# Kernel tuning notes

Measured on AMD Instinct MI355X. Metric: run time of the kernel, lower is better.

The kernel has to match this reference:

```python
import jax, jax.numpy as jnp
import numpy as np

N = 16384   # points (batch=1, divisible by patch_size so padding is identity)
C = 512     # channels
H = 8       # num_heads
K = 1024    # patch_size
G = 48      # voxel grid extent
EPS = 1e-5
SCALE = (C // H) ** -0.5


def setup_inputs() -> dict:
    rng = np.random.default_rng(0)
    # unique occupied voxels
    flat = rng.choice(G ** 3, size=N, replace=False)
    gx = flat // (G * G); gy = (flat // G) % G; gz = flat % G
    coords = np.stack([gx, gy, gz], 1).astype(np.int64)
    # occupancy LUT on padded grid -> neighbor index per 3x3x3 kernel offset (-1 = empty)
    lut = -np.ones(((G + 2) ** 3,), np.int64)
    def flt(c):
        return ((c[:, 0] + 1) * (G + 2) + (c[:, 1] + 1)) * (G + 2) + (c[:, 2] + 1)
    lut[flt(coords)] = np.arange(N)
    offs = np.array([[dx, dy, dz] for dx in (-1, 0, 1) for dy in (-1, 0, 1) for dz in (-1, 0, 1)], np.int64)
    nbr = np.stack([lut[flt(coords + o)] for o in offs], 1)  # [N,27]
    # Morton (z-order) serialization order
    def spread(v):
        v = v.astype(np.int64); r = np.zeros_like(v)
        for b in range(6):
            r |= ((v >> b) & 1) << (3 * b)
        return r
    code = (spread(gx) << 2) | (spread(gy) << 1) | spread(gz)
    order = np.argsort(code, kind='stable').astype(np.int32)

    key = jax.random.key(0)
    ks = jax.random.split(key, 8)
    s = 0.02
    p = lambda k, shape: jax.random.normal(k, shape, jnp.float32) * s
    return dict(
        feat=jax.random.normal(ks[0], (N, C), jnp.float32),
        neighbor_idx=jnp.asarray(nbr, jnp.int32),
        order=jnp.asarray(order, jnp.int32),
        cpe_w=p(ks[1], (27, C, C)), cpe_b=jnp.zeros((C,), jnp.float32),
        cpe_lin_w=p(ks[2], (C, C)), cpe_lin_b=jnp.zeros((C,), jnp.float32),
        cpe_ln_g=jnp.ones((C,), jnp.float32), cpe_ln_b=jnp.zeros((C,), jnp.float32),
        ln1_g=jnp.ones((C,), jnp.float32), ln1_b=jnp.zeros((C,), jnp.float32),
        qkv_w=p(ks[3], (3 * C, C)), qkv_b=jnp.zeros((3 * C,), jnp.float32),
        proj_w=p(ks[4], (C, C)), proj_b=jnp.zeros((C,), jnp.float32),
        ln2_g=jnp.ones((C,), jnp.float32), ln2_b=jnp.zeros((C,), jnp.float32),
        fc1_w=p(ks[5], (4 * C, C)), fc1_b=jnp.zeros((4 * C,), jnp.float32),
        fc2_w=p(ks[6], (C, 4 * C)), fc2_b=jnp.zeros((C,), jnp.float32),
    )


def _ln(x, g, b):
    m = x.mean(-1, keepdims=True)
    v = ((x - m) ** 2).mean(-1, keepdims=True)
    return (x - m) * jax.lax.rsqrt(v + EPS) * g + b


def _block(feat, neighbor_idx, order, cpe_w, cpe_b, cpe_lin_w, cpe_lin_b,
           cpe_ln_g, cpe_ln_b, ln1_g, ln1_b, qkv_w, qkv_b, proj_w, proj_b,
           ln2_g, ln2_b, fc1_w, fc1_b, fc2_w, fc2_b):
    # ---- CPE: SubMConv3d(3x3x3) -> Linear -> LayerNorm, residual ----
    valid = neighbor_idx >= 0
    idx = jnp.maximum(neighbor_idx, 0)
    h = jnp.zeros_like(feat)
    for kk in range(27):  # fixed kernel volume
        g = jnp.where(valid[:, kk:kk + 1], feat[idx[:, kk]], 0.0)
        h = h + g @ cpe_w[kk].T
    h = h + cpe_b
    h = h @ cpe_lin_w.T + cpe_lin_b
    h = _ln(h, cpe_ln_g, cpe_ln_b)
    feat = feat + h
    # ---- Serialized windowed attention (pre-norm, residual) ----
    x = _ln(feat, ln1_g, ln1_b)
    qkv = (x @ qkv_w.T + qkv_b)[order]                 # gather by serialized order
    qkv = qkv.reshape(N // K, K, 3, H, C // H)         # [P,K,3,H,hd]
    q = qkv[:, :, 0].transpose(0, 2, 1, 3)             # [P,H,K,hd]
    k = qkv[:, :, 1].transpose(0, 2, 1, 3)
    v = qkv[:, :, 2].transpose(0, 2, 1, 3)
    attn = jax.nn.softmax(jnp.einsum('phkd,phjd->phkj', q * SCALE, k), axis=-1)
    o = jnp.einsum('phkj,phjd->phkd', attn, v).transpose(0, 2, 1, 3).reshape(N, C)
    inverse = jnp.argsort(order)                       # scatter back
    o = o[inverse] @ proj_w.T + proj_b
    feat = feat + o
    # ---- MLP (pre-norm, residual) ----
    x = _ln(feat, ln2_g, ln2_b)
    x = jax.nn.gelu(x @ fc1_w.T + fc1_b, approximate=False)
    x = x @ fc2_w.T + fc2_b
    return feat + x


def reference(feat, neighbor_idx, order, cpe_w, cpe_b, cpe_lin_w, cpe_lin_b,
              cpe_ln_g, cpe_ln_b, ln1_g, ln1_b, qkv_w, qkv_b, proj_w, proj_b,
              ln2_g, ln2_b, fc1_w, fc1_b, fc2_w, fc2_b):
    return _block(feat, neighbor_idx, order, cpe_w, cpe_b, cpe_lin_w, cpe_lin_b,
                  cpe_ln_g, cpe_ln_b, ln1_g, ln1_b, qkv_w, qkv_b, proj_w, proj_b,
                  ln2_g, ln2_b, fc1_w, fc1_b, fc2_w, fc2_b)
```

## Files before the change

kernel.cpp:

```cpp
#include <hip/hip_runtime.h>
#include <math.h>

typedef unsigned short u16;
typedef unsigned int u32;
typedef unsigned long long u64;
typedef __attribute__((ext_vector_type(8))) short short8;
typedef __attribute__((ext_vector_type(4))) float f32x4;

#define NPTS 16384
#define MAXP 98304
#define MAXTILE 768

__device__ __forceinline__ u16 f2bf(float f) {
  u32 u = __float_as_uint(f);
  u = (u + 0x7fffu + ((u >> 16) & 1u)) >> 16;
  return (u16)u;
}
__device__ __forceinline__ float bf2f(u16 u) {
  return __uint_as_float((u32)u << 16);
}

__device__ __forceinline__ void gl2lds16(const u16* g, u16* l) {
  __builtin_amdgcn_global_load_lds(
      (const __attribute__((address_space(1))) u32*)g,
      (__attribute__((address_space(3))) u32*)l, 16, 0, 0);
}

__device__ __forceinline__ float wredsum(float v) {
#pragma unroll
  for (int m = 1; m < 64; m <<= 1) v += __shfl_xor(v, m, 64);
  return v;
}

__global__ void cvt_comb(const float* __restrict__ feat,
                         const float* __restrict__ w0, const float* __restrict__ w1,
                         const float* __restrict__ w2, const float* __restrict__ w3,
                         const float* __restrict__ w4, const float* __restrict__ w5,
                         u16* __restrict__ dst) {
  const int i = blockIdx.x * 256 + threadIdx.x;
  if (i >= 4718720) return;
  ushort4 o;
  if (i < 2097280) {
    if (i < 2097152) {
      float4 v = ((const float4*)feat)[i];
      o.x = f2bf(v.x); o.y = f2bf(v.y); o.z = f2bf(v.z); o.w = f2bf(v.w);
    } else {
      o.x = 0; o.y = 0; o.z = 0; o.w = 0;
    }
  } else {
    const int j = i - 2097280;
    const float* s;
    int li;
    if (j < 1769472) { s = w0; li = j; }
    else if (j < 1835008) { s = w1; li = j - 1769472; }
    else if (j < 2031616) { s = w2; li = j - 1835008; }
    else if (j < 2097152) { s = w3; li = j - 2031616; }
    else if (j < 2359296) { s = w4; li = j - 2097152; }
    else { s = w5; li = j - 2359296; }
    float4 v = ((const float4*)s)[li];
    o.x = f2bf(v.x); o.y = f2bf(v.y); o.z = f2bf(v.z); o.w = f2bf(v.w);
  }
  ((ushort4*)dst)[i] = o;
}

__global__ void mkinv(const int* __restrict__ order, int* __restrict__ inv) {
  int i = blockIdx.x * 256 + threadIdx.x;
  if (i < NPTS) inv[order[i]] = i;
}

__global__ __launch_bounds__(256) void cpe_cnt(const int* __restrict__ nbr,
                                               int* __restrict__ wcnt) {
  const int wglob = blockIdx.x * 4 + (threadIdx.x >> 6);
  const int lane = threadIdx.x & 63;
  const int i = wglob * 64 + lane;
  const int* row = nbr + i * 27;
#pragma unroll 1
  for (int kk = 0; kk < 27; kk++) {
    const u64 m = __ballot(row[kk] >= 0);
    if (lane == 0) wcnt[wglob * 27 + kk] = (int)__popcll(m);
  }
}

__global__ __launch_bounds__(256) void cpe_plan(
    const int* __restrict__ wcnt, int* __restrict__ chunkoff,
    int* __restrict__ off, int* __restrict__ tkk, int* __restrict__ meta,
    int* __restrict__ pairj) {
  __shared__ int s_cnt[27], s_off[27], s_ts[27], s_tk[27];
  const int tid = threadIdx.x;
  if (tid < 27) {
    int run = 0;
#pragma unroll 1
    for (int c = 0; c < 256; c++) {
      chunkoff[c * 27 + tid] = run;
      run += wcnt[c * 27 + tid];
    }
    s_cnt[tid] = run;
  }
  __syncthreads();
  if (tid == 0) {
    int pos = 0, t = 0;
#pragma unroll 1
    for (int kk = 0; kk < 27; kk++) {
      s_off[kk] = pos;
      off[kk] = pos;
      int tk = (s_cnt[kk] + 127) >> 7;
      if (pos + tk * 128 > MAXP) tk = (MAXP - pos) >> 7;
      s_ts[kk] = t;
      s_tk[kk] = tk;
      t += tk;
      pos += tk * 128;
    }
    meta[0] = t;
  }
  __syncthreads();
#pragma unroll 1
  for (int kk = 0; kk < 27; kk++) {
    const int ts = s_ts[kk], tk = s_tk[kk];
    for (int u = tid; u < tk; u += 256) tkk[ts + u] = kk;
    const int base = s_off[kk], total = s_cnt[kk], padded = tk * 128;
    for (int p2 = total + tid; p2 < padded; p2 += 256) pairj[base + p2] = NPTS;
  }
}

__global__ __launch_bounds__(256) void cpe_scat(
    const int* __restrict__ nbr, const int* __restrict__ chunkoff,
    const int* __restrict__ off, int* __restrict__ pairj,
    int* __restrict__ pairpos) {
  const int wglob = blockIdx.x * 4 + (threadIdx.x >> 6);
  const int lane = threadIdx.x & 63;
  const int i = wglob * 64 + lane;
  const int* row = nbr + i * 27;
  const u64 below = (1ull << lane) - 1ull;
#pragma unroll 1
  for (int kk = 0; kk < 27; kk++) {
    const int v = row[kk];
    const bool valid = v >= 0;
    const u64 m = __ballot(valid);
    int pp = -1;
    if (valid) {
      const int t = off[kk] + chunkoff[wglob * 27 + kk] + (int)__popcll(m & below);
      if (t < MAXP) { pairj[t] = v; pp = t; }
    }
    pairpos[i * 27 + kk] = pp;
  }
}

__global__ __launch_bounds__(256, 2) void gemm_pair(
    const u16* __restrict__ Abase, const u16* __restrict__ Bw,
    const int* __restrict__ meta, const int* __restrict__ tkk,
    const int* __restrict__ pairj, u16* __restrict__ outp) {
  const int L = blockIdx.x;
  const int tile = (L >> 5) * 8 + (L & 7);
  const int n0b = (L >> 3) & 3;
  if (tile >= meta[0]) return;
  __shared__ __align__(16) u16 sA[128 * 32];
  __shared__ __align__(16) u16 sB[128 * 32];
  const int tid = threadIdx.x;
  const int wave = tid >> 6, lane = tid & 63;
  const int quad = lane >> 4, tl = lane & 15;
  const int wr = wave >> 1, wc = wave & 1;
  const int p0 = tile * 128, n0 = n0b * 128;
  const int kk = tkk[tile];
  const int srow = lane >> 2, scol = lane & 3;

  int r[2]; int ca[2];
#pragma unroll
  for (int o = 0; o < 2; o++) {
    r[o] = wave * 32 + o * 16 + srow;
    const int sw = (r[o] + (r[o] >> 2)) & 3;
    ca[o] = (scol ^ sw) * 8;
  }
  const int j0 = pairj[p0 + r[0]];
  const int j1 = pairj[p0 + r[1]];
  const u16* a0 = Abase + (size_t)j0 * 512 + ca[0];
  const u16* a1 = Abase + (size_t)j1 * 512 + ca[1];
  const u16* b0 = Bw + (size_t)kk * 262144 + (size_t)(n0 + r[0]) * 512 + ca[0];
  const u16* b1 = Bw + (size_t)kk * 262144 + (size_t)(n0 + r[1]) * 512 + ca[1];
  u16* ldsA0 = &sA[(wave * 32) * 32];
  u16* ldsA1 = &sA[(wave * 32 + 16) * 32];
  u16* ldsB0 = &sB[(wave * 32) * 32];
  u16* ldsB1 = &sB[(wave * 32 + 16) * 32];

  f32x4 acc[4][4] = {};
#pragma unroll 1
  for (int kc = 0; kc < 512; kc += 32) {
    __syncthreads();
    gl2lds16(a0 + kc, ldsA0);
    gl2lds16(b0 + kc, ldsB0);
    gl2lds16(a1 + kc, ldsA1);
    gl2lds16(b1 + kc, ldsB1);
    __syncthreads();
    short8 fa[4], fb[4];
#pragma unroll
    for (int i = 0; i < 4; i++) {
      const int ra = wr * 64 + i * 16 + tl;
      fa[i] = *(const short8*)&sA[ra * 32 + ((quad ^ ((ra + (ra >> 2)) & 3)) * 8)];
      const int rb = wc * 64 + i * 16 + tl;
      fb[i] = *(const short8*)&sB[rb * 32 + ((quad ^ ((rb + (rb >> 2)) & 3)) * 8)];
    }
#pragma unroll
    for (int i = 0; i < 4; i++)
#pragma unroll
      for (int j = 0; j < 4; j++)
        acc[i][j] = __builtin_amdgcn_mfma_f32_16x16x32_bf16(fa[i], fb[j], acc[i][j], 0, 0, 0);
  }

#pragma unroll
  for (int i = 0; i < 4; i++) {
    const int pB = p0 + wr * 64 + i * 16 + quad * 4;
#pragma unroll
    for (int j = 0; j < 4; j++) {
      const int n = n0 + wc * 64 + j * 16 + tl;
      f32x4 c = acc[i][j];
#pragma unroll
      for (int rr = 0; rr < 4; rr++)
        outp[(size_t)(pB + rr) * 512 + n] = f2bf(c[rr]);
    }
  }
}

__global__ __launch_bounds__(256, 4) void cpe_reduce(
    const u16* __restrict__ outp, const int* __restrict__ pairpos,
    const float* __restrict__ bias, u16* __restrict__ h) {
  const int wave = threadIdx.x >> 6, lane = threadIdx.x & 63;
  const int i = blockIdx.x * 4 + wave;
  const int c = lane * 8;
  float acc[8];
  const float4 b0 = *(const float4*)(bias + c);
  const float4 b1 = *(const float4*)(bias + c + 4);
  acc[0] = b0.x; acc[1] = b0.y; acc[2] = b0.z; acc[3] = b0.w;
  acc[4] = b1.x; acc[5] = b1.y; acc[6] = b1.z; acc[7] = b1.w;
  const int* pp = pairpos + i * 27;
#pragma unroll 1
  for (int kk = 0; kk < 27; kk++) {
    const int pos = pp[kk];
    if (pos >= 0) {
      const u16* row = outp + (size_t)pos * 512 + c;
      ushort4 u0 = *(const ushort4*)row;
      ushort4 u1 = *(const ushort4*)(row + 4);
      acc[0] += bf2f(u0.x); acc[1] += bf2f(u0.y);
      acc[2] += bf2f(u0.z); acc[3] += bf2f(u0.w);
      acc[4] += bf2f(u1.x); acc[5] += bf2f(u1.y);
      acc[6] += bf2f(u1.z); acc[7] += bf2f(u1.w);
    }
  }
  ushort4 o0, o1;
  o0.x = f2bf(acc[0]); o0.y = f2bf(acc[1]); o0.z = f2bf(acc[2]); o0.w = f2bf(acc[3]);
  o1.x = f2bf(acc[4]); o1.y = f2bf(acc[5]); o1.z = f2bf(acc[6]); o1.w = f2bf(acc[7]);
  *(ushort4*)(h + (size_t)i * 512 + c) = o0;
  *(ushort4*)(h + (size_t)i * 512 + c + 4) = o1;
}

__global__ __launch_bounds__(256) void vtrans(const u16* __restrict__ vr,
                                              u16* __restrict__ vt) {
  __shared__ u16 t[64 * 72];
  const int bid = blockIdx.x;
  const int ph = bid >> 4, jt = bid & 15;
  const u16* src = vr + (size_t)ph * 65536 + jt * 64 * 64;
  u16* dst = vt + (size_t)ph * 65536 + jt * 64;
  const int tid = threadIdx.x;
  {
    const int j = tid >> 2, d0 = (tid & 3) * 16;
    uint4 w0 = *(const uint4*)(src + j * 64 + d0);
    uint4 w1 = *(const uint4*)(src + j * 64 + d0 + 8);
    *(uint4*)&t[j * 72 + d0] = w0;
    *(uint4*)&t[j * 72 + d0 + 8] = w1;
  }
  __syncthreads();
  {
    const int dr = tid >> 2, j0 = (tid & 3) * 16;
    u16 tmp[16];
#pragma unroll
    for (int e = 0; e < 16; e++) tmp[e] = t[(j0 + e) * 72 + dr];
    *(uint4*)(dst + (size_t)dr * 1024 + j0) = *(uint4*)&tmp[0];
    *(uint4*)(dst + (size_t)dr * 1024 + j0 + 8) = *(uint4*)&tmp[8];
  }
}

enum { EP_BF16 = 0, EP_QKV = 2, EP_RES = 3, EP_GELU = 4 };

template <int EP>
__global__ __launch_bounds__(256, 2) void gemm_nt(
    const u16* __restrict__ A, const u16* __restrict__ B, int M, int N, int K,
    const float* __restrict__ bias, float* __restrict__ outf,
    u16* __restrict__ outb, const float* __restrict__ res,
    const int* __restrict__ inv, u16* __restrict__ oq, u16* __restrict__ okk,
    u16* __restrict__ ov) {
  __shared__ __align__(16) u16 sA[128 * 32];
  __shared__ __align__(16) u16 sB[128 * 32];
  const int tid = threadIdx.x;
  const int wave = tid >> 6, lane = tid & 63;
  const int quad = lane >> 4, tl = lane & 15;
  const int wr = wave >> 1, wc = wave & 1;
  const int m0 = blockIdx.x * 128, n0 = blockIdx.y * 128;
  const int srow = lane >> 2, scol = lane & 3;

  f32x4 acc[4][4] = {};

  for (int kt = 0; kt < K; kt += 32) {
    __syncthreads();
#pragma unroll
    for (int o = 0; o < 2; o++) {
      const int r = wave * 32 + o * 16 + srow;
      const int sw = (r + (r >> 2)) & 3;
      const int ca = (scol ^ sw) * 8;
      gl2lds16(A + (size_t)(m0 + r) * K + kt + ca, &sA[(wave * 32 + o * 16) * 32]);
      gl2lds16(B + (size_t)(n0 + r) * K + kt + ca, &sB[(wave * 32 + o * 16) * 32]);
    }
    __syncthreads();
    short8 fa[4], fb[4];
#pragma unroll
    for (int i = 0; i < 4; i++) {
      const int ra = wr * 64 + i * 16 + tl;
      fa[i] = *(const short8*)&sA[ra * 32 + ((quad ^ ((ra + (ra >> 2)) & 3)) * 8)];
      const int rb = wc * 64 + i * 16 + tl;
      fb[i] = *(const short8*)&sB[rb * 32 + ((quad ^ ((rb + (rb >> 2)) & 3)) * 8)];
    }
#pragma unroll
    for (int i = 0; i < 4; i++)
#pragma unroll
      for (int j = 0; j < 4; j++)
        acc[i][j] = __builtin_amdgcn_mfma_f32_16x16x32_bf16(fa[i], fb[j], acc[i][j], 0, 0, 0);
  }

#pragma unroll
  for (int i = 0; i < 4; i++) {
    const int mB = m0 + wr * 64 + i * 16 + quad * 4;
#pragma unroll
    for (int j = 0; j < 4; j++) {
      const int n = n0 + wc * 64 + j * 16 + tl;
      const float bv = bias[n];
      f32x4 c = acc[i][j];
#pragma unroll
      for (int r = 0; r < 4; r++) {
        const int m = mB + r;
        float v = c[r] + bv;
        if (EP == EP_BF16) {
          outb[(size_t)m * N + n] = f2bf(v);
        } else if (EP == EP_RES) {
          outf[(size_t)m * N + n] = v + res[(size_t)m * N + n];
        } else if (EP == EP_GELU) {
          float g = 0.5f * v * (1.0f + erff(v * 0.70710678118654752f));
          outb[(size_t)m * N + n] = f2bf(g);
        } else if (EP == EP_QKV) {
          const int s = n >> 9, hh = (n >> 6) & 7, d = n & 63;
          const int pos = inv[m];
          const size_t base = (size_t)((pos >> 10) * 8 + hh) * 65536;
          const int jj = pos & 1023;
          if (s == 0) oq[base + (size_t)jj * 64 + d] = f2bf(v * 0.125f);
          else if (s == 1) okk[base + (size_t)jj * 64 + d] = f2bf(v);
          else ov[base + (size_t)jj * 64 + d] = f2bf(v);
        }
      }
    }
  }
}

__global__ __launch_bounds__(256, 2) void attn(
    const u16* __restrict__ qs, const u16* __restrict__ kk_s,
    const u16* __restrict__ vts, const int* __restrict__ order,
    u16* __restrict__ obf) {
  __shared__ __align__(16) u16 Qt[128 * 64];
  __shared__ __align__(16) u16 Kt[64 * 64];
  __shared__ __align__(16) u16 Vt[64 * 64];
  __shared__ __align__(16) u16 Pl[4][32 * 72];
  const int tid = threadIdx.x;
  const int wave = tid >> 6, lane = tid & 63;
  const int quad = lane >> 4, tl = lane & 15;
  const int bid = blockIdx.x;
  const int qt = bid >> 7, ph = bid & 127;
  const int p = ph >> 3, h = ph & 7;
  const size_t base = (size_t)ph * 65536;

  {
    const u16* Qg = qs + base + qt * 8192;
#pragma unroll
    for (int i = 0; i < 4; i++) {
      const int op = wave * 4 + i;
      const int r = op * 8 + (lane >> 3);
      const int c8 = ((lane & 7) ^ (r & 7)) * 8;
      gl2lds16(Qg + r * 64 + c8, &Qt[op * 512]);
    }
  }

  float ls[2][4] = {};
  f32x4 acco[2][4] = {};

  for (int kt = 0; kt < 16; kt++) {
    __syncthreads();
    const u16* Kg = kk_s + base + kt * 4096;
    const u16* Vg = vts + base + kt * 64;
#pragma unroll
    for (int i = 0; i < 2; i++) {
      const int op = wave * 2 + i;
      const int r = op * 8 + (lane >> 3);
      const int c8 = ((lane & 7) ^ (r & 7)) * 8;
      gl2lds16(Kg + r * 64 + c8, &Kt[op * 512]);
      gl2lds16(Vg + r * 1024 + c8, &Vt[op * 512]);
    }
    __syncthreads();

    f32x4 accs[2][4] = {};
#pragma unroll
    for (int kd = 0; kd < 2; kd++) {
      short8 qa[2], kb[4];
#pragma unroll
      for (int a = 0; a < 2; a++) {
        const int r = wave * 32 + a * 16 + tl;
        const int oct = (kd * 4 + quad) ^ (r & 7);
        qa[a] = *(const short8*)&Qt[r * 64 + oct * 8];
      }
#pragma unroll
      for (int b = 0; b < 4; b++) {
        const int r = b * 16 + tl;
        const int oct = (kd * 4 + quad) ^ (r & 7);
        kb[b] = *(const short8*)&Kt[r * 64 + oct * 8];
      }
#pragma unroll
      for (int a = 0; a < 2; a++)
#pragma unroll
        for (int b = 0; b < 4; b++)
          accs[a][b] = __builtin_amdgcn_mfma_f32_16x16x32_bf16(qa[a], kb[b], accs[a][b], 0, 0, 0);
    }

    u16* plw = &Pl[wave][0];
#pragma unroll
    for (int a = 0; a < 2; a++)
#pragma unroll
      for (int c = 0; c < 4; c++) {
#pragma unroll
        for (int r = 0; r < 4; r++) {
          const float pe = __expf(accs[a][c][r]);
          accs[a][c][r] = pe;
          ls[a][r] += pe;
          plw[(a * 16 + quad * 4 + r) * 72 + c * 16 + tl] = f2bf(pe);
        }
      }

#pragma unroll
    for (int k2 = 0; k2 < 2; k2++) {
      short8 pa[2], vb[4];
#pragma unroll
      for (int a = 0; a < 2; a++)
        pa[a] = *(const short8*)&plw[(a * 16 + tl) * 72 + k2 * 32 + quad * 8];
#pragma unroll
      for (int b = 0; b < 4; b++) {
        const int rb = b * 16 + tl;
        vb[b] = *(const short8*)&Vt[rb * 64 + (((k2 * 4 + quad) ^ (rb & 7)) * 8)];
      }
#pragma unroll
      for (int a = 0; a < 2; a++)
#pragma unroll
        for (int b = 0; b < 4; b++)
          acco[a][b] = __builtin_amdgcn_mfma_f32_16x16x32_bf16(pa[a], vb[b], acco[a][b], 0, 0, 0);
    }
  }

#pragma unroll
  for (int a = 0; a < 2; a++)
#pragma unroll
    for (int r = 0; r < 4; r++) {
#pragma unroll
      for (int mk = 1; mk < 16; mk <<= 1) ls[a][r] += __shfl_xor(ls[a][r], mk, 64);
    }

  const int q0 = p * 1024 + qt * 128 + wave * 32;
#pragma unroll
  for (int a = 0; a < 2; a++)
#pragma unroll
    for (int r = 0; r < 4; r++) {
      const int orig = order[q0 + a * 16 + quad * 4 + r];
      const float il = 1.0f / ls[a][r];
#pragma unroll
      for (int b = 0; b < 4; b++)
        obf[(size_t)orig * 512 + h * 64 + b * 16 + tl] = f2bf(acco[a][b][r] * il);
    }
}

__global__ __launch_bounds__(256, 4) void ln_fuse1(
    const u16* __restrict__ h2, const float* __restrict__ feat,
    const float* __restrict__ cg, const float* __restrict__ cb,
    const float* __restrict__ g1, const float* __restrict__ b1,
    float* __restrict__ feat1, u16* __restrict__ xbf) {
  const int wave = threadIdx.x >> 6, lane = threadIdx.x & 63;
  const size_t row = (size_t)blockIdx.x * 4 + wave;
  const int c0 = lane * 4, c1 = 256 + lane * 4;
  const u16* hr = h2 + row * 512;
  ushort4 ha = *(const ushort4*)(hr + c0);
  ushort4 hb = *(const ushort4*)(hr + c1);
  float h[8];
  h[0] = bf2f(ha.x); h[1] = bf2f(ha.y); h[2] = bf2f(ha.z); h[3] = bf2f(ha.w);
  h[4] = bf2f(hb.x); h[5] = bf2f(hb.y); h[6] = bf2f(hb.z); h[7] = bf2f(hb.w);
  float s = 0.0f, q = 0.0f;
#pragma unroll
  for (int i = 0; i < 8; i++) { s += h[i]; q += h[i] * h[i]; }
  s = wredsum(s); q = wredsum(q);
  const float mean = s * (1.0f / 512.0f);
  const float var = q * (1.0f / 512.0f) - mean * mean;
  const float rs = rsqrtf(var + 1e-5f);
  float4 ga = *(const float4*)(cg + c0), gb = *(const float4*)(cg + c1);
  float4 ba = *(const float4*)(cb + c0), bb = *(const float4*)(cb + c1);
  const float* fr = feat + row * 512;
  float4 fa = *(const float4*)(fr + c0), fb = *(const float4*)(fr + c1);
  float f[8];
  f[0] = fa.x + (h[0] - mean) * rs * ga.x + ba.x;
  f[1] = fa.y + (h[1] - mean) * rs * ga.y + ba.y;
  f[2] = fa.z + (h[2] - mean) * rs * ga.z + ba.z;
  f[3] = fa.w + (h[3] - mean) * rs * ga.w + ba.w;
  f[4] = fb.x + (h[4] - mean) * rs * gb.x + bb.x;
  f[5] = fb.y + (h[5] - mean) * rs * gb.y + bb.y;
  f[6] = fb.z + (h[6] - mean) * rs * gb.z + bb.z;
  f[7] = fb.w + (h[7] - mean) * rs * gb.w + bb.w;
  float* f1r = feat1 + row * 512;
  *(float4*)(f1r + c0) = make_float4(f[0], f[1], f[2], f[3]);
  *(float4*)(f1r + c1) = make_float4(f[4], f[5], f[6], f[7]);
  float s2 = 0.0f, q2 = 0.0f;
#pragma unroll
  for (int i = 0; i < 8; i++) { s2 += f[i]; q2 += f[i] * f[i]; }
  s2 = wredsum(s2); q2 = wredsum(q2);
  const float mean2 = s2 * (1.0f / 512.0f);
  const float var2 = q2 * (1.0f / 512.0f) - mean2 * mean2;
  const float rs2 = rsqrtf(var2 + 1e-5f);
  float4 g1a = *(const float4*)(g1 + c0), g1b = *(const float4*)(g1 + c1);
  float4 b1a = *(const float4*)(b1 + c0), b1b = *(const float4*)(b1 + c1);
  ushort4 o0, o1;
  o0.x = f2bf((f[0] - mean2) * rs2 * g1a.x + b1a.x);
  o0.y = f2bf((f[1] - mean2) * rs2 * g1a.y + b1a.y);
  o0.z = f2bf((f[2] - mean2) * rs2 * g1a.z + b1a.z);
  o0.w = f2bf((f[3] - mean2) * rs2 * g1a.w + b1a.w);
  o1.x = f2bf((f[4] - mean2) * rs2 * g1b.x + b1b.x);
  o1.y = f2bf((f[5] - mean2) * rs2 * g1b.y + b1b.y);
  o1.z = f2bf((f[6] - mean2) * rs2 * g1b.z + b1b.z);
  o1.w = f2bf((f[7] - mean2) * rs2 * g1b.w + b1b.w);
  *(ushort4*)(xbf + row * 512 + c0) = o0;
  *(ushort4*)(xbf + row * 512 + c1) = o1;
}

__global__ __launch_bounds__(256, 4) void ln_only(
    const float* __restrict__ x, const float* __restrict__ g,
    const float* __restrict__ b_, u16* __restrict__ o) {
  const int wave = threadIdx.x >> 6, lane = threadIdx.x & 63;
  const size_t row = (size_t)blockIdx.x * 4 + wave;
  const int c0 = lane * 4, c1 = 256 + lane * 4;
  const float* xr = x + row * 512;
  float4 a = *(const float4*)(xr + c0);
  float4 b = *(const float4*)(xr + c1);
  float s = a.x + a.y + a.z + a.w + b.x + b.y + b.z + b.w;
  float q = a.x * a.x + a.y * a.y + a.z * a.z + a.w * a.w +
            b.x * b.x + b.y * b.y + b.z * b.z + b.w * b.w;
  s = wredsum(s); q = wredsum(q);
  const float mean = s * (1.0f / 512.0f);
  const float var = q * (1.0f / 512.0f) - mean * mean;
  const float rs = rsqrtf(var + 1e-5f);
  float4 ga = *(const float4*)(g + c0), gb = *(const float4*)(g + c1);
  float4 ba = *(const float4*)(b_ + c0), bb = *(const float4*)(b_ + c1);
  ushort4 o0, o1;
  o0.x = f2bf((a.x - mean) * rs * ga.x + ba.x);
  o0.y = f2bf((a.y - mean) * rs * ga.y + ba.y);
  o0.z = f2bf((a.z - mean) * rs * ga.z + ba.z);
  o0.w = f2bf((a.w - mean) * rs * ga.w + ba.w);
  o1.x = f2bf((b.x - mean) * rs * gb.x + bb.x);
  o1.y = f2bf((b.y - mean) * rs * gb.y + bb.y);
  o1.z = f2bf((b.z - mean) * rs * gb.z + bb.z);
  o1.w = f2bf((b.w - mean) * rs * gb.w + bb.w);
  *(ushort4*)(o + row * 512 + c0) = o0;
  *(ushort4*)(o + row * 512 + c1) = o1;
}

extern "C" void kernel_launch(void* const* d_in, const int* in_sizes, int n_in,
                              void* d_out, int out_size, void* d_ws, size_t ws_size,
                              hipStream_t stream) {
  (void)in_sizes; (void)n_in; (void)out_size; (void)ws_size;
  const float* feat = (const float*)d_in[0];
  const int* nbr = (const int*)d_in[1];
  const int* order = (const int*)d_in[2];
  const float* cpe_w = (const float*)d_in[3];
  const float* cpe_b = (const float*)d_in[4];
  const float* cpe_lin_w = (const float*)d_in[5];
  const float* cpe_lin_b = (const float*)d_in[6];
  const float* cpe_ln_g = (const float*)d_in[7];
  const float* cpe_ln_b = (const float*)d_in[8];
  const float* ln1_g = (const float*)d_in[9];
  const float* ln1_b = (const float*)d_in[10];
  const float* qkv_w = (const float*)d_in[11];
  const float* qkv_b = (const float*)d_in[12];
  const float* proj_w = (const float*)d_in[13];
  const float* proj_b = (const float*)d_in[14];
  const float* ln2_g = (const float*)d_in[15];
  const float* ln2_b = (const float*)d_in[16];
  const float* fc1_w = (const float*)d_in[17];
  const float* fc1_b = (const float*)d_in[18];
  const float* fc2_w = (const float*)d_in[19];
  const float* fc2_b = (const float*)d_in[20];
  float* out = (float*)d_out;

  char* ws = (char*)d_ws;
  size_t off = 0;
  auto alloc = [&](size_t bytes) {
    char* p = ws + off;
    off += (bytes + 255) & ~(size_t)255;
    return p;
  };
  u16* featbf = (u16*)alloc((size_t)(NPTS + 1) * 512 * 2);
  u16* w_cpe = (u16*)alloc((size_t)27 * 512 * 512 * 2);
  u16* w_cl = (u16*)alloc((size_t)512 * 512 * 2);
  u16* w_qkv = (u16*)alloc((size_t)1536 * 512 * 2);
  u16* w_proj = (u16*)alloc((size_t)512 * 512 * 2);
  u16* w_fc1 = (u16*)alloc((size_t)2048 * 512 * 2);
  u16* w_fc2 = (u16*)alloc((size_t)512 * 2048 * 2);
  u16* hbf = (u16*)alloc((size_t)NPTS * 512 * 2);
  char* big = alloc((size_t)NPTS * 2048 * 2);
  float* feat1 = (float*)alloc((size_t)NPTS * 512 * 4);
  int* inv = (int*)alloc((size_t)NPTS * 4);
  int* offs = (int*)alloc(27 * 4);
  int* meta = (int*)alloc(256);
  int* tkk = (int*)alloc((size_t)(MAXTILE + 1) * 4);
  int* pairj = (int*)alloc((size_t)MAXP * 4);
  int* pairpos = (int*)alloc((size_t)NPTS * 27 * 4);
  int* wcnt = (int*)alloc((size_t)256 * 27 * 4);
  int* chunkoff = (int*)alloc((size_t)256 * 27 * 4);

  u16* out_pair = (u16*)big;
  u16* h2 = (u16*)big;
  u16* qsb = (u16*)big;
  u16* ksb = qsb + (size_t)NPTS * 512;
  u16* vrow = ksb + (size_t)NPTS * 512;
  u16* vtb = vrow + (size_t)NPTS * 512;
  u16* tbf = (u16*)big;
  u16* xbf = hbf;
  u16* obf = hbf;
  u16* x2bf = featbf;

  cvt_comb<<<dim3(18433), dim3(256), 0, stream>>>(feat, cpe_w, cpe_lin_w, qkv_w,
                                                  proj_w, fc1_w, fc2_w, featbf);
  mkinv<<<dim3(NPTS / 256), dim3(256), 0, stream>>>(order, inv);

  cpe_cnt<<<dim3(64), dim3(256), 0, stream>>>(nbr, wcnt);
  cpe_plan<<<dim3(1), dim3(256), 0, stream>>>(wcnt, chunkoff, offs, tkk, meta, pairj);
  cpe_scat<<<dim3(64), dim3(256), 0, stream>>>(nbr, chunkoff, offs, pairj, pairpos);
  gemm_pair<<<dim3(MAXTILE * 4), dim3(256), 0, stream>>>(featbf, w_cpe, meta, tkk,
                                                         pairj, out_pair);
  cpe_reduce<<<dim3(NPTS / 4), dim3(256), 0, stream>>>(out_pair, pairpos, cpe_b, hbf);

  gemm_nt<EP_BF16><<<dim3(128, 4), dim3(256), 0, stream>>>(
      hbf, w_cl, NPTS, 512, 512, cpe_lin_b, nullptr, h2, nullptr, nullptr,
      nullptr, nullptr, nullptr);
  ln_fuse1<<<dim3(NPTS / 4), dim3(256), 0, stream>>>(
      h2, feat, cpe_ln_g, cpe_ln_b, ln1_g, ln1_b, feat1, xbf);
  gemm_nt<EP_QKV><<<dim3(128, 12), dim3(256), 0, stream>>>(
      xbf, w_qkv, NPTS, 1536, 512, qkv_b, nullptr, nullptr, nullptr, inv,
      qsb, ksb, vrow);
  vtrans<<<dim3(2048), dim3(256), 0, stream>>>(vrow, vtb);
  attn<<<dim3(1024), dim3(256), 0, stream>>>(qsb, ksb, vtb, order, obf);
  gemm_nt<EP_RES><<<dim3(128, 4), dim3(256), 0, stream>>>(
      obf, w_proj, NPTS, 512, 512, proj_b, out, nullptr, feat1, nullptr,
      nullptr, nullptr, nullptr);
  ln_only<<<dim3(NPTS / 4), dim3(256), 0, stream>>>(out, ln2_g, ln2_b, x2bf);
  gemm_nt<EP_GELU><<<dim3(128, 16), dim3(256), 0, stream>>>(
      x2bf, w_fc1, NPTS, 2048, 512, fc1_b, nullptr, tbf, nullptr, nullptr,
      nullptr, nullptr, nullptr);
  gemm_nt<EP_RES><<<dim3(128, 4), dim3(256), 0, stream>>>(
      tbf, w_fc2, NPTS, 512, 2048, fc2_b, out, nullptr, out, nullptr,
      nullptr, nullptr, nullptr);
}
```

Measured before the change: 596.2 us.

## Halve tile sizes for attention and N=512 GEMMs to raise block count

Adds a 64x128-tile GEMM variant used for the cpe_lin, proj and fc2 GEMMs, doubling their grid to 1024 blocks. The attention kernel now handles 64 queries per block instead of 128, doubling blocks to 2048, with lower LDS and register use and a higher occupancy bound. The aim is to fill the GPU's many CUs better, since 512 blocks underfill the machine. The cost is reloading K/V tiles twice as often, lower arithmetic intensity per block, and a single-buffered k-loop with small 32-wide steps in the new GEMM.

```diff
diff --git a/kernel.cpp b/kernel.cpp
--- a/kernel.cpp
+++ b/kernel.cpp
@@ -356,14 +356,86 @@
   }
 }
 
-__global__ __launch_bounds__(256, 2) void attn(
+template <int EP>
+__global__ __launch_bounds__(256) void gemm_nt64(
+    const u16* __restrict__ A, const u16* __restrict__ B, int M, int N, int K,
+    const float* __restrict__ bias, float* __restrict__ outf,
+    u16* __restrict__ outb, const float* __restrict__ res) {
+  __shared__ __align__(16) u16 sA[64 * 32];
+  __shared__ __align__(16) u16 sB[128 * 32];
+  const int tid = threadIdx.x;
+  const int wave = tid >> 6, lane = tid & 63;
+  const int quad = lane >> 4, tl = lane & 15;
+  const int wr = wave >> 1, wc = wave & 1;
+  const int m0 = blockIdx.x * 64, n0 = blockIdx.y * 128;
+  const int srow = lane >> 2, scol = lane & 3;
+
+  f32x4 acc[2][4] = {};
+
+  for (int kt = 0; kt < K; kt += 32) {
+    __syncthreads();
+    {
+      const int r = wave * 16 + srow;
+      const int sw = (r + (r >> 2)) & 3;
+      const int ca = (scol ^ sw) * 8;
+      gl2lds16(A + (size_t)(m0 + r) * K + kt + ca, &sA[(wave * 16) * 32]);
+    }
+#pragma unroll
+    for (int o = 0; o < 2; o++) {
+      const int r = wave * 32 + o * 16 + srow;
+      const int sw = (r + (r >> 2)) & 3;
+      const int ca = (scol ^ sw) * 8;
+      gl2lds16(B + (size_t)(n0 + r) * K + kt + ca, &sB[(wave * 32 + o * 16) * 32]);
+    }
+    __syncthreads();
+    short8 fa[2], fb[4];
+#pragma unroll
+    for (int i = 0; i < 2; i++) {
+      const int ra = wr * 32 + i * 16 + tl;
+      fa[i] = *(const short8*)&sA[ra * 32 + ((quad ^ ((ra + (ra >> 2)) & 3)) * 8)];
+    }
+#pragma unroll
+    for (int j = 0; j < 4; j++) {
+      const int rb = wc * 64 + j * 16 + tl;
+      fb[j] = *(const short8*)&sB[rb * 32 + ((quad ^ ((rb + (rb >> 2)) & 3)) * 8)];
+    }
+#pragma unroll
+    for (int i = 0; i < 2; i++)
+#pragma unroll
+      for (int j = 0; j < 4; j++)
+        acc[i][j] = __builtin_amdgcn_mfma_f32_16x16x32_bf16(fa[i], fb[j], acc[i][j], 0, 0, 0);
+  }
+
+#pragma unroll
+  for (int i = 0; i < 2; i++) {
+    const int mB = m0 + wr * 32 + i * 16 + quad * 4;
+#pragma unroll
+    for (int j = 0; j < 4; j++) {
+      const int n = n0 + wc * 64 + j * 16 + tl;
+      const float bv = bias[n];
+      f32x4 c = acc[i][j];
+#pragma unroll
+      for (int r = 0; r < 4; r++) {
+        const int m = mB + r;
+        float v = c[r] + bv;
+        if (EP == EP_BF16) {
+          outb[(size_t)m * N + n] = f2bf(v);
+        } else if (EP == EP_RES) {
+          outf[(size_t)m * N + n] = v + res[(size_t)m * N + n];
+        }
+      }
+    }
+  }
+}
+
+__global__ __launch_bounds__(256, 4) void attn(
     const u16* __restrict__ qs, const u16* __restrict__ kk_s,
     const u16* __restrict__ vts, const int* __restrict__ order,
     u16* __restrict__ obf) {
-  __shared__ __align__(16) u16 Qt[128 * 64];
+  __shared__ __align__(16) u16 Qt[64 * 64];
   __shared__ __align__(16) u16 Kt[64 * 64];
   __shared__ __align__(16) u16 Vt[64 * 64];
-  __shared__ __align__(16) u16 Pl[4][32 * 72];
+  __shared__ __align__(16) u16 Pl[4][16 * 72];
   const int tid = threadIdx.x;
   const int wave = tid >> 6, lane = tid & 63;
   const int quad = lane >> 4, tl = lane & 15;
@@ -373,18 +445,18 @@
   const size_t base = (size_t)ph * 65536;
 
   {
-    const u16* Qg = qs + base + qt * 8192;
-#pragma unroll
-    for (int i = 0; i < 4; i++) {
-      const int op = wave * 4 + i;
+    const u16* Qg = qs + base + qt * 4096;
+#pragma unroll
+    for (int i = 0; i < 2; i++) {
+      const int op = wave * 2 + i;
       const int r = op * 8 + (lane >> 3);
       const int c8 = ((lane & 7) ^ (r & 7)) * 8;
       gl2lds16(Qg + r * 64 + c8, &Qt[op * 512]);
     }
   }
 
-  float ls[2][4] = {};
-  f32x4 acco[2][4] = {};
+  float ls[4] = {};
+  f32x4 acco[4] = {};
 
   for (int kt = 0; kt < 16; kt++) {
     __syncthreads();
@@ -400,15 +472,14 @@
     }
     __syncthreads();
 
-    f32x4 accs[2][4] = {};
+    f32x4 accs[4] = {};
 #pragma unroll
     for (int kd = 0; kd < 2; kd++) {
-      short8 qa[2], kb[4];
-#pragma unroll
-      for (int a = 0; a < 2; a++) {
-        const int r = wave * 32 + a * 16 + tl;
+      short8 qa, kb[4];
+      {
+        const int r = wave * 16 + tl;
         const int oct = (kd * 4 + quad) ^ (r & 7);
-        qa[a] = *(const short8*)&Qt[r * 64 + oct * 8];
+        qa = *(const short8*)&Qt[r * 64 + oct * 8];
       }
 #pragma unroll
       for (int b = 0; b < 4; b++) {
@@ -417,64 +488,52 @@
         kb[b] = *(const short8*)&Kt[r * 64 + oct * 8];
       }
 #pragma unroll
-      for (int a = 0; a < 2; a++)
-#pragma unroll
-        for (int b = 0; b < 4; b++)
-          accs[a][b] = __builtin_amdgcn_mfma_f32_16x16x32_bf16(qa[a], kb[b], accs[a][b], 0, 0, 0);
+      for (int b = 0; b < 4; b++)
+        accs[b] = __builtin_amdgcn_mfma_f32_16x16x32_bf16(qa, kb[b], accs[b], 0, 0, 0);
     }
 
     u16* plw = &Pl[wave][0];
 #pragma unroll
-    for (int a = 0; a < 2; a++)
-#pragma unroll
-      for (int c = 0; c < 4; c++) {
-#pragma unroll
-        for (int r = 0; r < 4; r++) {
-          const float pe = __expf(accs[a][c][r]);
-          accs[a][c][r] = pe;
-          ls[a][r] += pe;
-          plw[(a * 16 + quad * 4 + r) * 72 + c * 16 + tl] = f2bf(pe);
-        }
+    for (int c = 0; c < 4; c++) {
+#pragma unroll
+      for (int r = 0; r < 4; r++) {
+        const float pe = __expf(accs[c][r]);
+        accs[c][r] = pe;
+        ls[r] += pe;
+        plw[(quad * 4 + r) * 72 + c * 16 + tl] = f2bf(pe);
       }
+    }
 
 #pragma unroll
     for (int k2 = 0; k2 < 2; k2++) {
-      short8 pa[2], vb[4];
-#pragma unroll
-      for (int a = 0; a < 2; a++)
-        pa[a] = *(const short8*)&plw[(a * 16 + tl) * 72 + k2 * 32 + quad * 8];
+      short8 pa, vb[4];
+      pa = *(const short8*)&plw[tl * 72 + k2 * 32 + quad * 8];
 #pragma unroll
       for (int b = 0; b < 4; b++) {
         const int rb = b * 16 + tl;
         vb[b] = *(const short8*)&Vt[rb * 64 + (((k2 * 4 + quad) ^ (rb & 7)) * 8)];
       }
 #pragma unroll
-      for (int a = 0; a < 2; a++)
-#pragma unroll
-        for (int b = 0; b < 4; b++)
-          acco[a][b] = __builtin_amdgcn_mfma_f32_16x16x32_bf16(pa[a], vb[b], acco[a][b], 0, 0, 0);
-    }
-  }
-
-#pragma unroll
-  for (int a = 0; a < 2; a++)
-#pragma unroll
-    for (int r = 0; r < 4; r++) {
-#pragma unroll
-      for (int mk = 1; mk < 16; mk <<= 1) ls[a][r] += __shfl_xor(ls[a][r], mk, 64);
-    }
-
-  const int q0 = p * 1024 + qt * 128 + wave * 32;
-#pragma unroll
-  for (int a = 0; a < 2; a++)
-#pragma unroll
-    for (int r = 0; r < 4; r++) {
-      const int orig = order[q0 + a * 16 + quad * 4 + r];
-      const float il = 1.0f / ls[a][r];
-#pragma unroll
       for (int b = 0; b < 4; b++)
-        obf[(size_t)orig * 512 + h * 64 + b * 16 + tl] = f2bf(acco[a][b][r] * il);
-    }
+        acco[b] = __builtin_amdgcn_mfma_f32_16x16x32_bf16(pa, vb[b], acco[b], 0, 0, 0);
+    }
+  }
+
+#pragma unroll
+  for (int r = 0; r < 4; r++) {
+#pragma unroll
+    for (int mk = 1; mk < 16; mk <<= 1) ls[r] += __shfl_xor(ls[r], mk, 64);
+  }
+
+  const int q0 = p * 1024 + qt * 64 + wave * 16;
+#pragma unroll
+  for (int r = 0; r < 4; r++) {
+    const int orig = order[q0 + quad * 4 + r];
+    const float il = 1.0f / ls[r];
+#pragma unroll
+    for (int b = 0; b < 4; b++)
+      obf[(size_t)orig * 512 + h * 64 + b * 16 + tl] = f2bf(acco[b][r] * il);
+  }
 }
 
 __global__ __launch_bounds__(256, 4) void ln_fuse1(
@@ -642,24 +701,21 @@
                                                          pairj, out_pair);
   cpe_reduce<<<dim3(NPTS / 4), dim3(256), 0, stream>>>(out_pair, pairpos, cpe_b, hbf);
 
-  gemm_nt<EP_BF16><<<dim3(128, 4), dim3(256), 0, stream>>>(
-      hbf, w_cl, NPTS, 512, 512, cpe_lin_b, nullptr, h2, nullptr, nullptr,
-      nullptr, nullptr, nullptr);
+  gemm_nt64<EP_BF16><<<dim3(256, 4), dim3(256), 0, stream>>>(
+      hbf, w_cl, NPTS, 512, 512, cpe_lin_b, nullptr, h2, nullptr);
   ln_fuse1<<<dim3(NPTS / 4), dim3(256), 0, stream>>>(
       h2, feat, cpe_ln_g, cpe_ln_b, ln1_g, ln1_b, feat1, xbf);
   gemm_nt<EP_QKV><<<dim3(128, 12), dim3(256), 0, stream>>>(
       xbf, w_qkv, NPTS, 1536, 512, qkv_b, nullptr, nullptr, nullptr, inv,
       qsb, ksb, vrow);
   vtrans<<<dim3(2048), dim3(256), 0, stream>>>(vrow, vtb);
-  attn<<<dim3(1024), dim3(256), 0, stream>>>(qsb, ksb, vtb, order, obf);
-  gemm_nt<EP_RES><<<dim3(128, 4), dim3(256), 0, stream>>>(
-      obf, w_proj, NPTS, 512, 512, proj_b, out, nullptr, feat1, nullptr,
-      nullptr, nullptr, nullptr);
+  attn<<<dim3(2048), dim3(256), 0, stream>>>(qsb, ksb, vtb, order, obf);
+  gemm_nt64<EP_RES><<<dim3(256, 4), dim3(256), 0, stream>>>(
+      obf, w_proj, NPTS, 512, 512, proj_b, out, nullptr, feat1);
   ln_only<<<dim3(NPTS / 4), dim3(256), 0, stream>>>(out, ln2_g, ln2_b, x2bf);
   gemm_nt<EP_GELU><<<dim3(128, 16), dim3(256), 0, stream>>>(
       x2bf, w_fc1, NPTS, 2048, 512, fc1_b, nullptr, tbf, nullptr, nullptr,
       nullptr, nullptr, nullptr);
-  gemm_nt<EP_RES><<<dim3(128, 4), dim3(256), 0, stream>>>(
-      tbf, w_fc2, NPTS, 512, 2048, fc2_b, out, nullptr, out, nullptr,
-      nullptr, nullptr, nullptr);
-}
+  gemm_nt64<EP_RES><<<dim3(256, 4), dim3(256), 0, stream>>>(
+      tbf, w_fc2, NPTS, 512, 2048, fc2_b, out, nullptr, out);
+}
```

Measured after the change: 613.9 us. 3.0% more time.
